# Performance work log

Hardware: AMD Instinct MI355X
Metric: run time of the kernel (lower is better)

Reference implementation:

```python
import jax, jax.numpy as jnp
import numpy as np

TOP_K_FRACTION = 0.1


def setup_inputs() -> dict:
    key = jax.random.key(0)
    k1, k2, k3 = jax.random.split(key, 3)
    B, H, S, D = 2, 12, 1024, 64
    q = jax.random.normal(k1, (B, H, S, D), dtype=jnp.float32)
    k = jax.random.normal(k2, (B, H, S, D), dtype=jnp.float32)
    v = jax.random.normal(k3, (B, H, S, D), dtype=jnp.float32)
    mask = jnp.zeros((B, 1, 1, S), dtype=jnp.float32)
    return {"q": q, "k": k, "v": v, "mask": mask}


def reference(q, k, v, mask):
    B, H, S, D = q.shape
    k_precise = max(1, int(S * TOP_K_FRACTION))
    # binary (sign) approximation of attention scores; detached like torch
    q_bin = jnp.sign(jax.lax.stop_gradient(q))
    k_bin = jnp.sign(jax.lax.stop_gradient(k))
    approx_scores = jnp.einsum('bhsd,bhtd->bhst', q_bin, k_bin) / D  # [B,H,S,S]
    _, topk_idx = jax.lax.top_k(approx_scores, k_precise)  # [B,H,S,kp]
    # gather top-k keys/values per query: [B,H,S,kp,D]
    k_gathered = jnp.take_along_axis(k[:, :, None, :, :], topk_idx[..., None], axis=3)
    v_gathered = jnp.take_along_axis(v[:, :, None, :, :], topk_idx[..., None], axis=3)
    scale = np.float32(1.0 / np.sqrt(D))
    precise_scores = jnp.einsum('bhsd,bhskd->bhsk', q, k_gathered) * scale
    # gather mask along key positions: mask [B,1,1,S] -> [B,H,S,kp]
    mask_gathered = jnp.take_along_axis(
        jnp.broadcast_to(mask, (B, H, S, S)), topk_idx, axis=-1)
    precise_scores = precise_scores + mask_gathered
    precise_probs = jax.nn.softmax(precise_scores, axis=-1)
    attn_output = jnp.einsum('bhsk,bhskd->bhsd', precise_probs, v_gathered)
    return attn_output
```

## Files before the change

### kernel.cpp

```cpp
#include <hip/hip_runtime.h>
#include <hip/hip_fp16.h>
#include <cstdint>

#define BB 2
#define HH 12
#define SS 1024
#define DD 64
#define KP 102
#define CHK 64
#define KROW 72
#define SELW 17

typedef _Float16 half8v  __attribute__((ext_vector_type(8)));
typedef float    float4v __attribute__((ext_vector_type(4)));
typedef unsigned long long u64;

__device__ __forceinline__ int mbcnt64(u64 m) {
    return (int)__builtin_amdgcn_mbcnt_hi((unsigned)(m >> 32),
               __builtin_amdgcn_mbcnt_lo((unsigned)(m & 0xffffffffull), 0u));
}
template <int CTRL>
__device__ __forceinline__ float dpp_f(float x) {
    return __builtin_bit_cast(float,
        __builtin_amdgcn_update_dpp(0, __builtin_bit_cast(int, x), CTRL, 0xF, 0xF, false));
}
__device__ __forceinline__ float row16_sum(float x) {
    x += dpp_f<0xB1>(x);
    x += dpp_f<0x4E>(x);
    x += dpp_f<0x141>(x);
    x += dpp_f<0x140>(x);
    return x;
}

__global__ __launch_bounds__(256) void pack_kernel(
    const float* __restrict__ k, const float* __restrict__ v,
    u64* __restrict__ kbits, _Float16* __restrict__ kh, _Float16* __restrict__ vT)
{
    __shared__ __align__(16) _Float16 vt_lds[DD * KROW];
    const int tid  = (int)threadIdx.x;
    const int w    = tid >> 6;
    const int lane = tid & 63;
    const int bh = (int)blockIdx.x >> 4;
    const int t0 = ((int)blockIdx.x & 15) * 64;

    const float* kbase = k + ((size_t)bh * SS + t0) * DD;
    const float* vbase = v + ((size_t)bh * SS + t0) * DD;
    #pragma unroll 1
    for (int i = 0; i < 16; ++i) {
        int rl = w * 16 + i;
        float kv = kbase[rl * DD + lane];
        float vv = vbase[rl * DD + lane];
        u64 km = __ballot(kv > 0.0f);
        kh[((size_t)bh * SS + t0 + rl) * DD + lane] = (_Float16)kv;
        vt_lds[lane * KROW + rl] = (_Float16)vv;
        if (lane == 0) kbits[(size_t)bh * SS + t0 + rl] = km;
    }
    __syncthreads();
    #pragma unroll
    for (int it = 0; it < 2; ++it) {
        int s = tid + it * 256;
        int d = s >> 3, c8 = s & 7;
        *(half8v*)(vT + ((size_t)bh * DD + d) * SS + t0 + c8 * 8) =
            *(const half8v*)(&vt_lds[d * KROW + c8 * 8]);
    }
}

__global__ __launch_bounds__(256) void select_kernel(
    const float* __restrict__ q, const u64* __restrict__ kbits,
    u64* __restrict__ selbm)
{
    const int tid  = (int)threadIdx.x;
    const int w    = tid >> 6;
    const int lane = tid & 63;
    const int qbase = (int)blockIdx.x * 16 + w * 4;
    const int bh    = qbase >> 10;

    const u64* kb = kbits + (size_t)bh * SS;
    u64 kbreg[16];
    #pragma unroll
    for (int j = 0; j < 16; ++j) kbreg[j] = kb[j * 64 + lane];

    #pragma unroll 1
    for (int qq = 0; qq < 4; ++qq) {
        const int qid = qbase + qq;
        float qv = q[(size_t)qid * DD + lane];
        u64 qm = __ballot(qv > 0.0f);
        int pbin[16];
        #pragma unroll
        for (int j = 0; j < 16; ++j) pbin[j] = (int)__popcll(qm ^ kbreg[j]);
        #define COUNT_LE(P, OUTC)                                      \
            { int _c = 0;                                              \
              _Pragma("unroll")                                        \
              for (int j = 0; j < 16; ++j)                             \
                  _c += (int)__popcll(__ballot(pbin[j] <= (P)));       \
              (OUTC) = _c; }
        int P = 27, c, clt;
        COUNT_LE(P, c);
        if (c >= KP) {
            COUNT_LE(P - 1, clt);
            while (clt >= KP) { c = clt; --P; COUNT_LE(P - 1, clt); }
        } else {
            do { clt = c; ++P; COUNT_LE(P, c); } while (c < KP);
        }
        const int binP = P;
        const int need = KP - clt;
        #undef COUNT_LE
        u64 my_tm = 0; int tie_base = 0;
        #pragma unroll
        for (int j = 0; j < 16; ++j) {
            bool isGt  = pbin[j] < binP;
            bool isTie = (pbin[j] == binP);
            u64 tiem = __ballot(isTie);
            int rank = tie_base + mbcnt64(tiem);
            bool take = isGt || (isTie && rank < need);
            u64 tm = __ballot(take);
            if (lane == j) my_tm = tm;
            tie_base += (int)__popcll(tiem);
        }
        if (lane < 16) selbm[(size_t)qid * 16 + lane] = my_tm;
    }
}

__global__ __launch_bounds__(256, 2) void battn_kernel(
    const float* __restrict__ q, const _Float16* __restrict__ kh,
    const _Float16* __restrict__ vT, const float* __restrict__ mask,
    const u64* __restrict__ selbm, float* __restrict__ out)
{
    const int tid  = (int)threadIdx.x;
    const int w    = tid >> 6;
    const int lane = tid & 63;
    const int bh    = (int)blockIdx.x >> 4;
    const int qtile = (int)blockIdx.x & 15;
    const int bidx  = bh / HH;
    const int qr    = lane & 15;
    const int quad  = lane >> 4;

    __shared__ __align__(16) _Float16 K_lds[CHK * KROW];
    __shared__ __align__(16) _Float16 VT_lds[DD * KROW];
    __shared__ __align__(16) _Float16 P_lds[4][16 * KROW];
    __shared__ u64 sel[64 * SELW];

    #pragma unroll
    for (int it = 0; it < 4; ++it) {
        int s = tid + it * 256;
        int ql = s >> 4, j = s & 15;
        sel[ql * SELW + j] = selbm[((size_t)bh * SS + qtile * 64 + ql) * 16 + j];
    }

    const float* qblock = q + ((size_t)bh * SS + qtile * 64) * DD;
    half8v qa0, qa1;
    {
        const float* qf = qblock + (w * 16 + qr) * DD + quad * 8;
        #pragma unroll
        for (int j = 0; j < 8; ++j) {
            qa0[j] = (_Float16)(qf[j] * 0.125f);
            qa1[j] = (_Float16)(qf[32 + j] * 0.125f);
        }
    }

    const _Float16* khead  = kh + (size_t)bh * SS * DD;
    const _Float16* vthead = vT + (size_t)bh * DD * SS;
    const float*    mrow   = mask + (size_t)bidx * SS;
    const int s0 = tid, s1 = tid + 256;
    const int r0 = s0 >> 3, c0 = (s0 & 7) * 8;
    const int r1 = s1 >> 3, c1 = (s1 & 7) * 8;

    half8v kp0, kp1, vp0, vp1;
    kp0 = *(const half8v*)(khead + (size_t)(0 * CHK + r0) * DD + c0);
    kp1 = *(const half8v*)(khead + (size_t)(0 * CHK + r1) * DD + c1);
    vp0 = *(const half8v*)(vthead + (size_t)r0 * SS + 0 * CHK + c0);
    vp1 = *(const half8v*)(vthead + (size_t)r1 * SS + 0 * CHK + c1);

    float4v acc[4];
    #pragma unroll
    for (int dt = 0; dt < 4; ++dt) { acc[dt][0]=0.f; acc[dt][1]=0.f; acc[dt][2]=0.f; acc[dt][3]=0.f; }
    float lp[4] = {0.f, 0.f, 0.f, 0.f};

    #pragma unroll 1
    for (int ch = 0; ch < 16; ++ch) {
        __syncthreads();
        *(half8v*)(&K_lds[r0 * KROW + c0])  = kp0;
        *(half8v*)(&K_lds[r1 * KROW + c1])  = kp1;
        *(half8v*)(&VT_lds[r0 * KROW + c0]) = vp0;
        *(half8v*)(&VT_lds[r1 * KROW + c1]) = vp1;
        __syncthreads();

        if (ch < 15) {
            kp0 = *(const half8v*)(khead + (size_t)((ch + 1) * CHK + r0) * DD + c0);
            kp1 = *(const half8v*)(khead + (size_t)((ch + 1) * CHK + r1) * DD + c1);
            vp0 = *(const half8v*)(vthead + (size_t)r0 * SS + (ch + 1) * CHK + c0);
            vp1 = *(const half8v*)(vthead + (size_t)r1 * SS + (ch + 1) * CHK + c1);
        }

        #pragma unroll
        for (int nt = 0; nt < 4; ++nt) {
            const _Float16* klp = &K_lds[(nt * 16 + qr) * KROW + quad * 8];
            half8v b0 = *(const half8v*)klp;
            half8v b1 = *(const half8v*)(klp + 32);
            float4v cfr; cfr[0]=0.f; cfr[1]=0.f; cfr[2]=0.f; cfr[3]=0.f;
            cfr = __builtin_amdgcn_mfma_f32_16x16x32_f16(qa0, b0, cfr, 0, 0, 0);
            cfr = __builtin_amdgcn_mfma_f32_16x16x32_f16(qa1, b1, cfr, 0, 0, 0);
            const int tg = ch * CHK + nt * 16 + qr;
            const float mk = mrow[tg] - 4.0f;
            const int u32i = (tg >> 5) & 1;
            const int wj   = tg >> 6;
            #pragma unroll
            for (int r = 0; r < 4; ++r) {
                const int ql = w * 16 + quad * 4 + r;
                unsigned sm = ((const unsigned*)&sel[ql * SELW + wj])[u32i];
                float e = ((sm >> (tg & 31)) & 1u) ? __expf(cfr[r] + mk) : 0.0f;
                lp[r] += e;
                P_lds[w][(quad * 4 + r) * KROW + nt * 16 + qr] = (_Float16)e;
            }
        }

        half8v pa0 = *(const half8v*)(&P_lds[w][qr * KROW + quad * 8]);
        half8v pa1 = *(const half8v*)(&P_lds[w][qr * KROW + 32 + quad * 8]);
        #pragma unroll
        for (int dt = 0; dt < 4; ++dt) {
            const _Float16* vl = &VT_lds[(dt * 16 + qr) * KROW + quad * 8];
            acc[dt] = __builtin_amdgcn_mfma_f32_16x16x32_f16(pa0, *(const half8v*)vl,        acc[dt], 0, 0, 0);
            acc[dt] = __builtin_amdgcn_mfma_f32_16x16x32_f16(pa1, *(const half8v*)(vl + 32), acc[dt], 0, 0, 0);
        }
    }

    float rinv[4];
    #pragma unroll
    for (int r = 0; r < 4; ++r) rinv[r] = __frcp_rn(row16_sum(lp[r]));
    float* orow = out + ((size_t)bh * SS + qtile * 64 + w * 16) * DD;
    #pragma unroll
    for (int dt = 0; dt < 4; ++dt)
        #pragma unroll
        for (int r = 0; r < 4; ++r)
            orow[(quad * 4 + r) * DD + dt * 16 + qr] = acc[dt][r] * rinv[r];
}

extern "C" void kernel_launch(void* const* d_in, const int* in_sizes, int n_in,
                              void* d_out, int out_size, void* d_ws, size_t ws_size,
                              hipStream_t stream) {
    const float* q    = (const float*)d_in[0];
    const float* k    = (const float*)d_in[1];
    const float* v    = (const float*)d_in[2];
    const float* mask = (const float*)d_in[3];
    float* out = (float*)d_out;

    const int rows = BB * HH * SS;
    u64* kbits = (u64*)d_ws;
    _Float16* kh = (_Float16*)((char*)d_ws + (size_t)rows * sizeof(u64));
    _Float16* vT = kh + (size_t)rows * DD;
    u64* selbm = (u64*)(vT + (size_t)rows * DD);

    pack_kernel<<<rows / 64, 256, 0, stream>>>(k, v, kbits, kh, vT);
    select_kernel<<<rows / 16, 256, 0, stream>>>(q, kbits, selbm);
    battn_kernel<<<BB * HH * (SS / 64), 256, 0, stream>>>(q, kh, vT, mask, selbm, out);
}
```

Measured before the change: 118.2 us.

## Split attention over two key halves and combine partial sums in a new kernel

The attention kernel now splits each query tile's key range into two halves processed by separate blocks, doubling the grid to 768 blocks. Each block writes unnormalized partial outputs and row sums to workspace, and a new combine kernel adds the two halves and normalizes. Selection bits are preloaded per chunk as 64-bit words, and launch bounds are raised to allow more resident blocks. This is meant to improve occupancy and parallelism across CUs, at the cost of an extra kernel launch and a partial-output round trip through global memory.

```diff
diff --git a/kernel.cpp b/kernel.cpp
--- a/kernel.cpp
+++ b/kernel.cpp
@@ -9,7 +9,7 @@
 #define KP 102
 #define CHK 64
 #define KROW 72
-#define SELW 17
+#define SELW 9
 
 typedef _Float16 half8v  __attribute__((ext_vector_type(8)));
 typedef float    float4v __attribute__((ext_vector_type(4)));
@@ -121,16 +121,19 @@
     }
 }
 
-__global__ __launch_bounds__(256, 2) void battn_kernel(
+__global__ __launch_bounds__(256, 4) void battn_kernel(
     const float* __restrict__ q, const _Float16* __restrict__ kh,
     const _Float16* __restrict__ vT, const float* __restrict__ mask,
-    const u64* __restrict__ selbm, float* __restrict__ out)
+    const u64* __restrict__ selbm, float* __restrict__ pO, float* __restrict__ pL)
 {
     const int tid  = (int)threadIdx.x;
     const int w    = tid >> 6;
     const int lane = tid & 63;
-    const int bh    = (int)blockIdx.x >> 4;
-    const int qtile = (int)blockIdx.x & 15;
+    const int ph    = (int)blockIdx.x;
+    const int half  = ph & 1;
+    const int qt    = ph >> 1;
+    const int bh    = qt >> 4;
+    const int qtile = qt & 15;
     const int bidx  = bh / HH;
     const int qr    = lane & 15;
     const int quad  = lane >> 4;
@@ -141,10 +144,11 @@
     __shared__ u64 sel[64 * SELW];
 
     #pragma unroll
-    for (int it = 0; it < 4; ++it) {
+    for (int it = 0; it < 2; ++it) {
         int s = tid + it * 256;
-        int ql = s >> 4, j = s & 15;
-        sel[ql * SELW + j] = selbm[((size_t)bh * SS + qtile * 64 + ql) * 16 + j];
+        int ql = s >> 3, j = s & 7;
+        sel[ql * SELW + j] =
+            selbm[((size_t)bh * SS + qtile * 64 + ql) * 16 + half * 8 + j];
     }
 
     const float* qblock = q + ((size_t)bh * SS + qtile * 64) * DD;
@@ -158,18 +162,18 @@
         }
     }
 
-    const _Float16* khead  = kh + (size_t)bh * SS * DD;
-    const _Float16* vthead = vT + (size_t)bh * DD * SS;
-    const float*    mrow   = mask + (size_t)bidx * SS;
+    const _Float16* khead  = kh + ((size_t)bh * SS + half * 512) * DD;
+    const _Float16* vthead = vT + (size_t)bh * DD * SS + half * 512;
+    const float*    mrow   = mask + (size_t)bidx * SS + half * 512;
     const int s0 = tid, s1 = tid + 256;
     const int r0 = s0 >> 3, c0 = (s0 & 7) * 8;
     const int r1 = s1 >> 3, c1 = (s1 & 7) * 8;
 
     half8v kp0, kp1, vp0, vp1;
-    kp0 = *(const half8v*)(khead + (size_t)(0 * CHK + r0) * DD + c0);
-    kp1 = *(const half8v*)(khead + (size_t)(0 * CHK + r1) * DD + c1);
-    vp0 = *(const half8v*)(vthead + (size_t)r0 * SS + 0 * CHK + c0);
-    vp1 = *(const half8v*)(vthead + (size_t)r1 * SS + 0 * CHK + c1);
+    kp0 = *(const half8v*)(khead + (size_t)r0 * DD + c0);
+    kp1 = *(const half8v*)(khead + (size_t)r1 * DD + c1);
+    vp0 = *(const half8v*)(vthead + (size_t)r0 * SS + c0);
+    vp1 = *(const half8v*)(vthead + (size_t)r1 * SS + c1);
 
     float4v acc[4];
     #pragma unroll
@@ -177,7 +181,7 @@
     float lp[4] = {0.f, 0.f, 0.f, 0.f};
 
     #pragma unroll 1
-    for (int ch = 0; ch < 16; ++ch) {
+    for (int ch = 0; ch < 8; ++ch) {
         __syncthreads();
         *(half8v*)(&K_lds[r0 * KROW + c0])  = kp0;
         *(half8v*)(&K_lds[r1 * KROW + c1])  = kp1;
@@ -185,12 +189,17 @@
         *(half8v*)(&VT_lds[r1 * KROW + c1]) = vp1;
         __syncthreads();
 
-        if (ch < 15) {
+        if (ch < 7) {
             kp0 = *(const half8v*)(khead + (size_t)((ch + 1) * CHK + r0) * DD + c0);
             kp1 = *(const half8v*)(khead + (size_t)((ch + 1) * CHK + r1) * DD + c1);
             vp0 = *(const half8v*)(vthead + (size_t)r0 * SS + (ch + 1) * CHK + c0);
             vp1 = *(const half8v*)(vthead + (size_t)r1 * SS + (ch + 1) * CHK + c1);
         }
+
+        u64 sw[4];
+        #pragma unroll
+        for (int r = 0; r < 4; ++r)
+            sw[r] = sel[(w * 16 + quad * 4 + r) * SELW + ch];
 
         #pragma unroll
         for (int nt = 0; nt < 4; ++nt) {
@@ -200,17 +209,13 @@
             float4v cfr; cfr[0]=0.f; cfr[1]=0.f; cfr[2]=0.f; cfr[3]=0.f;
             cfr = __builtin_amdgcn_mfma_f32_16x16x32_f16(qa0, b0, cfr, 0, 0, 0);
             cfr = __builtin_amdgcn_mfma_f32_16x16x32_f16(qa1, b1, cfr, 0, 0, 0);
-            const int tg = ch * CHK + nt * 16 + qr;
-            const float mk = mrow[tg] - 4.0f;
-            const int u32i = (tg >> 5) & 1;
-            const int wj   = tg >> 6;
+            const int tl = nt * 16 + qr;
+            const float mk = mrow[ch * CHK + tl] - 4.0f;
             #pragma unroll
             for (int r = 0; r < 4; ++r) {
-                const int ql = w * 16 + quad * 4 + r;
-                unsigned sm = ((const unsigned*)&sel[ql * SELW + wj])[u32i];
-                float e = ((sm >> (tg & 31)) & 1u) ? __expf(cfr[r] + mk) : 0.0f;
+                float e = ((sw[r] >> tl) & 1ull) ? __expf(cfr[r] + mk) : 0.0f;
                 lp[r] += e;
-                P_lds[w][(quad * 4 + r) * KROW + nt * 16 + qr] = (_Float16)e;
+                P_lds[w][(quad * 4 + r) * KROW + tl] = (_Float16)e;
             }
         }
 
@@ -224,15 +229,37 @@
         }
     }
 
-    float rinv[4];
-    #pragma unroll
-    for (int r = 0; r < 4; ++r) rinv[r] = __frcp_rn(row16_sum(lp[r]));
-    float* orow = out + ((size_t)bh * SS + qtile * 64 + w * 16) * DD;
+    #pragma unroll
+    for (int r = 0; r < 4; ++r) lp[r] = row16_sum(lp[r]);
+    if (qr == 0) {
+        float* plrow = pL + (size_t)ph * 64 + w * 16 + quad * 4;
+        plrow[0] = lp[0]; plrow[1] = lp[1]; plrow[2] = lp[2]; plrow[3] = lp[3];
+    }
+    float* porow = pO + (size_t)ph * 4096 + (size_t)(w * 16) * DD;
     #pragma unroll
     for (int dt = 0; dt < 4; ++dt)
         #pragma unroll
         for (int r = 0; r < 4; ++r)
-            orow[(quad * 4 + r) * DD + dt * 16 + qr] = acc[dt][r] * rinv[r];
+            porow[(quad * 4 + r) * DD + dt * 16 + qr] = acc[dt][r];
+}
+
+__global__ __launch_bounds__(256) void combine_kernel(
+    const float* __restrict__ pO, const float* __restrict__ pL,
+    float* __restrict__ out)
+{
+    const int idx4 = (int)(blockIdx.x * 256 + threadIdx.x);
+    const int flat = idx4 * 4;
+    const int qid  = flat >> 6;
+    const int d0   = flat & 63;
+    const int qt   = qid >> 6;
+    const int ql   = qid & 63;
+    const int p0   = qt * 2, p1 = qt * 2 + 1;
+    const float rinv = __frcp_rn(pL[(size_t)p0 * 64 + ql] + pL[(size_t)p1 * 64 + ql]);
+    float4v a = *(const float4v*)(pO + (size_t)p0 * 4096 + ql * 64 + d0);
+    float4v b = *(const float4v*)(pO + (size_t)p1 * 4096 + ql * 64 + d0);
+    float4v o; o[0] = (a[0]+b[0])*rinv; o[1] = (a[1]+b[1])*rinv;
+               o[2] = (a[2]+b[2])*rinv; o[3] = (a[3]+b[3])*rinv;
+    *(float4v*)(out + flat) = o;
 }
 
 extern "C" void kernel_launch(void* const* d_in, const int* in_sizes, int n_in,
@@ -245,12 +272,16 @@
     float* out = (float*)d_out;
 
     const int rows = BB * HH * SS;
-    u64* kbits = (u64*)d_ws;
-    _Float16* kh = (_Float16*)((char*)d_ws + (size_t)rows * sizeof(u64));
-    _Float16* vT = kh + (size_t)rows * DD;
-    u64* selbm = (u64*)(vT + (size_t)rows * DD);
+    char* ws = (char*)d_ws;
+    u64*      kbits = (u64*)ws;                          ws += (size_t)rows * 8;
+    _Float16* kh    = (_Float16*)ws;                     ws += (size_t)rows * DD * 2;
+    _Float16* vT    = (_Float16*)ws;                     ws += (size_t)rows * DD * 2;
+    u64*      selbm = (u64*)ws;                          ws += (size_t)rows * 16 * 8;
+    float*    pO    = (float*)ws;                        ws += (size_t)768 * 4096 * 4;
+    float*    pL    = (float*)ws;
 
     pack_kernel<<<rows / 64, 256, 0, stream>>>(k, v, kbits, kh, vT);
     select_kernel<<<rows / 16, 256, 0, stream>>>(q, kbits, selbm);
-    battn_kernel<<<BB * HH * (SS / 64), 256, 0, stream>>>(q, kh, vT, mask, selbm, out);
-}
+    battn_kernel<<<768, 256, 0, stream>>>(q, kh, vT, mask, selbm, pO, pL);
+    combine_kernel<<<rows * DD / 1024, 256, 0, stream>>>(pO, pL, out);
+}
```

After: 118.4 us. No clear change (+0.1%).
